# Kernel optimization log

Hardware: AMD Instinct MI355X
Metric: run time of the kernel (lower is better)

## Reference

```python
import jax, jax.numpy as jnp
import numpy as np

B, S, HID, USZ, PSZ, OUT = 128, 512, 768, 200, 200, 200
N_SENT = 16  # 16 sentences of 32 tokens; offsets row = [0,32,...,480,-1]


def setup_inputs() -> dict:
    key = jax.random.key(0)
    ks = jax.random.split(key, 8)
    H = jax.random.normal(ks[0], (B, S, HID), jnp.float32)
    u = jax.random.normal(ks[1], (B, USZ), jnp.float32)
    p = jax.random.normal(ks[2], (B, PSZ), jnp.float32)
    Wh = jax.random.normal(ks[3], (HID, OUT), jnp.float32) * 0.05
    Wu = jax.random.normal(ks[4], (USZ, OUT), jnp.float32) * 0.05
    Wp = jax.random.normal(ks[5], (PSZ, OUT), jnp.float32) * 0.05
    v = jax.random.normal(ks[6], (OUT,), jnp.float32) * 0.05
    b = jnp.zeros((OUT,), jnp.float32)  # torch buffer self.b = zeros
    # offsets: N_SENT sentence starts + trailing -1 sentinel -> [B, N_SENT+1]
    row = jnp.concatenate([jnp.arange(N_SENT, dtype=jnp.int32) * (S // N_SENT),
                           jnp.array([-1], jnp.int32)])
    sentence_offsets = jnp.tile(row[None, :], (B, 1))
    return {"H": H, "u": u, "p": p, "Wh": Wh, "Wu": Wu, "Wp": Wp,
            "v": v, "b": b, "sentence_offsets": sentence_offsets}


def reference(H, u, p, Wh, Wu, Wp, v, b, sentence_offsets):
    # Additive attention scores for every token: v . tanh(Wh H + Wu u + Wp p + b)
    Ht = jnp.einsum('bsh,ho->bso', H, Wh)                      # [B,S,OUT]
    ut = (u @ Wu)[:, None, :]                                  # [B,1,OUT]
    pt = (p @ Wp)[:, None, :]                                  # [B,1,OUT]
    scores = jnp.tanh(Ht + ut + pt + b) @ v                    # [B,S]

    Bsz, Sl, _ = H.shape
    beg = sentence_offsets[:, :-1]                             # [B,M]
    nxt = sentence_offsets[:, 1:]                              # [B,M]
    valid = beg != -1
    # faithful to torch: end = 512 if next==-1 else next-1 (off-by-one kept)
    end = jnp.where(nxt == -1, Sl, nxt - 1)
    t = jnp.arange(Sl)
    mask = valid[:, :, None] & (t[None, None, :] >= beg[:, :, None]) \
           & (t[None, None, :] < end[:, :, None])              # [B,M,S]

    neg_inf = jnp.float32(-jnp.inf)
    em = jnp.where(mask, scores[:, None, :], neg_inf)
    m = jnp.max(em, axis=-1, keepdims=True)
    w = jnp.exp(em - jnp.where(jnp.isfinite(m), m, 0.0)) * mask
    denom = jnp.sum(w, axis=-1, keepdims=True)
    alphas = w / jnp.where(denom > 0, denom, 1.0)              # ragged softmax
    # per-sentence weighted sum of H -> [B, M, HID] (invalid sentences = 0)
    return jnp.einsum('bms,bsh->bmh', alphas, H)
```

## Files before the change

kernel.cpp:

```cpp
#include <hip/hip_runtime.h>
#include <math.h>

#define Bn   128
#define Sn   512
#define HIDn 768
#define OUTn 200
#define MSEG 16
#define NPAD 224
#define NT   14
#define NTW  7
#define KIT  24
#define ROWS 32
#define PH   3
#define KPP  8

typedef __attribute__((ext_vector_type(8))) short short8;
typedef __attribute__((ext_vector_type(4))) float f32x4;

#define GL2LDS(gp, lp) __builtin_amdgcn_global_load_lds(                  \
    (const __attribute__((address_space(1))) void*)(gp),                  \
    (__attribute__((address_space(3))) void*)(lp), 16, 0, 0)

static __device__ inline unsigned short f2bf(float f) {
  union { float f; unsigned u; } v; v.f = f;
  unsigned r = v.u + 0x7FFFu + ((v.u >> 16) & 1u);
  return (unsigned short)(r >> 16);
}

static __device__ inline float fast_tanh(float x) {
  float t = fabsf(x);
  float e = __expf(-2.f * t);
  float r = (1.f - e) * __builtin_amdgcn_rcpf(1.f + e);
  return copysignf(r, x);
}

__global__ __launch_bounds__(256) void setup_kernel(
    const float* __restrict__ Wh, const float* __restrict__ v,
    unsigned short* __restrict__ WhF, float* __restrict__ vP) {
  int idx = blockIdx.x * 256 + threadIdx.x;
  if (blockIdx.x == 0 && threadIdx.x < NPAD)
    vP[threadIdx.x] = (threadIdx.x < OUTn) ? v[threadIdx.x] : 0.f;
  if (idx < NPAD * HIDn) {
    int n = idx / HIDn;
    int k = idx - n * HIDn;
    float val = (n < OUTn) ? Wh[(size_t)k * OUTn + n] : 0.f;
    size_t d = ((size_t)(k >> 5) * NT + (n >> 4)) * 512
             + ((k >> 3) & 3) * 128 + (n & 15) * 8 + (k & 7);
    WhF[d] = f2bf(val);
  }
}

__global__ __launch_bounds__(256) void bias_kernel(
    const float* __restrict__ u, const float* __restrict__ p,
    const float* __restrict__ Wu, const float* __restrict__ Wp,
    const float* __restrict__ bvec, float* __restrict__ biasP) {
  int b = blockIdx.x;
  __shared__ float ul[OUTn], pl[OUTn];
  int tid = threadIdx.x;
  if (tid < OUTn) { ul[tid] = u[b * OUTn + tid]; pl[tid] = p[b * OUTn + tid]; }
  __syncthreads();
  if (tid < NPAD) {
    float s0 = 0.f, s1 = 0.f;
    if (tid < OUTn) {
      s0 = bvec[tid];
      for (int k = 0; k < OUTn; k += 2) {
        s0 += ul[k] * Wu[k * OUTn + tid] + pl[k] * Wp[k * OUTn + tid];
        s1 += ul[k + 1] * Wu[(k + 1) * OUTn + tid] + pl[k + 1] * Wp[(k + 1) * OUTn + tid];
      }
    }
    biasP[(size_t)b * NPAD + tid] = s0 + s1;
  }
}

__global__ __launch_bounds__(256) void fused_kernel(
    const float* __restrict__ H, const unsigned short* __restrict__ WhF,
    const float* __restrict__ biasP, const float* __restrict__ vP,
    const int* __restrict__ offs, float* __restrict__ out) {
  __shared__ float As[2][KPP * 1024];
  __shared__ float scp[2][ROWS];
  __shared__ float o_l[4][HIDn];

  int tid = threadIdx.x, wave = tid >> 6, lane = tid & 63;
  int quad = lane >> 4, l16 = lane & 15;
  int mh = wave >> 1, nh = wave & 1;
  int bid = blockIdx.x;
  int b = bid >> 4;
  int seg = bid & 15;
  int s0 = seg << 5;

  const float* Hblk = H + (size_t)(b * Sn + s0) * HIDn;

  int rloc = lane >> 3;
  int csrc = (lane & 7) ^ (rloc & 7);
  const float* Hst = Hblk + (size_t)rloc * HIDn + csrc * 4;

#define STAGE(ph, bf)                                                        \
  {                                                                          \
    _Pragma("unroll")                                                        \
    for (int t = 0; t < 8; ++t) {                                            \
      int i_ = wave * 8 + t;                                                 \
      int ks_ = i_ >> 2, qt_ = i_ & 3;                                       \
      GL2LDS(Hst + (size_t)(qt_ * 8) * HIDn + ((ph) * KPP + ks_) * 32,       \
             &As[bf][ks_ * 1024 + qt_ * 256]);                               \
    }                                                                        \
  }

  f32x4 acc[NTW];
#pragma unroll
  for (int j = 0; j < NTW; ++j) acc[j] = (f32x4){0.f, 0.f, 0.f, 0.f};

  const short8* Bw = (const short8*)WhF + lane;
  int row = mh * 16 + l16;
  int slot0 = (2 * quad) ^ (l16 & 7);

  STAGE(0, 0);
  __syncthreads();

#pragma unroll
  for (int ph = 0; ph < PH; ++ph) {
    int bf = ph & 1;
#pragma unroll
    for (int ks = 0; ks < KPP; ++ks) {
      int kk = ph * KPP + ks;
      short8 bfr[NTW];
#pragma unroll
      for (int j = 0; j < NTW; ++j)
        bfr[j] = Bw[(kk * NT + nh * NTW + j) * 64];
      if (ks == 2 && ph + 1 < PH) STAGE(ph + 1, bf ^ 1);
      const float* Ab = &As[bf][ks * 1024 + row * 32];
      float4 h0 = *(const float4*)(Ab + slot0 * 4);
      float4 h1 = *(const float4*)(Ab + (slot0 ^ 1) * 4);
      short8 a;
      a[0] = f2bf(h0.x); a[1] = f2bf(h0.y); a[2] = f2bf(h0.z); a[3] = f2bf(h0.w);
      a[4] = f2bf(h1.x); a[5] = f2bf(h1.y); a[6] = f2bf(h1.z); a[7] = f2bf(h1.w);
#pragma unroll
      for (int j = 0; j < NTW; ++j)
        acc[j] = __builtin_amdgcn_mfma_f32_16x16x32_bf16(a, bfr[j], acc[j], 0, 0, 0);
    }
    __syncthreads();
  }

  {
    const float* bp = biasP + (size_t)b * NPAD + nh * (NTW * 16) + l16;
    const float* vp = vP + nh * (NTW * 16) + l16;
    float bv[NTW], vv[NTW];
#pragma unroll
    for (int j = 0; j < NTW; ++j) { bv[j] = bp[j * 16]; vv[j] = vp[j * 16]; }
#pragma unroll
    for (int r = 0; r < 4; ++r) {
      float s = 0.f;
#pragma unroll
      for (int j = 0; j < NTW; ++j)
        s += fast_tanh(acc[j][r] + bv[j]) * vv[j];
      s += __shfl_xor(s, 1); s += __shfl_xor(s, 2);
      s += __shfl_xor(s, 4); s += __shfl_xor(s, 8);
      if (l16 == 0) scp[nh][mh * 16 + quad * 4 + r] = s;
    }
  }
  __syncthreads();

  int beg = offs[b * (MSEG + 1) + seg];
  int nxt = offs[b * (MSEG + 1) + seg + 1];
  bool valid = (beg != -1);
  int end = (nxt == -1) ? Sn : nxt - 1;

  float x = -INFINITY;
  if (lane < 32) {
    int rw = s0 + lane;
    if (valid && rw >= beg && rw < end)
      x = scp[0][lane] + scp[1][lane];
  }
  float mx = x;
  mx = fmaxf(mx, __shfl_xor(mx, 1));  mx = fmaxf(mx, __shfl_xor(mx, 2));
  mx = fmaxf(mx, __shfl_xor(mx, 4));  mx = fmaxf(mx, __shfl_xor(mx, 8));
  mx = fmaxf(mx, __shfl_xor(mx, 16)); mx = fmaxf(mx, __shfl_xor(mx, 32));
  float mm = (mx > -1e30f) ? mx : 0.f;
  float e = __expf(x - mm);
  float ls = e;
  ls += __shfl_xor(ls, 1);  ls += __shfl_xor(ls, 2);
  ls += __shfl_xor(ls, 4);  ls += __shfl_xor(ls, 8);
  ls += __shfl_xor(ls, 16); ls += __shfl_xor(ls, 32);
  float inv = (ls > 0.f) ? 1.f / ls : 0.f;
  float av = e * inv;

  float af[8];
#pragma unroll
  for (int i = 0; i < 8; ++i) af[i] = __shfl(av, wave * 8 + i);

  const float4* Hrow = (const float4*)(H + (size_t)(b * Sn + s0 + wave * 8) * HIDn);
  float4 o0 = {0,0,0,0}, o1 = {0,0,0,0}, o2 = {0,0,0,0};
#pragma unroll
  for (int i = 0; i < 8; ++i) {
    const float4* hp = Hrow + (size_t)i * (HIDn / 4);
    float4 h0 = hp[lane], h1 = hp[lane + 64], h2 = hp[lane + 128];
    float a = af[i];
    o0.x += a * h0.x; o0.y += a * h0.y; o0.z += a * h0.z; o0.w += a * h0.w;
    o1.x += a * h1.x; o1.y += a * h1.y; o1.z += a * h1.z; o1.w += a * h1.w;
    o2.x += a * h2.x; o2.y += a * h2.y; o2.z += a * h2.z; o2.w += a * h2.w;
  }
  {
    float4* ol = (float4*)o_l[wave];
    ol[lane] = o0; ol[lane + 64] = o1; ol[lane + 128] = o2;
  }
  __syncthreads();

  if (tid < 192) {
    const float4* p0 = (const float4*)o_l[0];
    const float4* p1 = (const float4*)o_l[1];
    const float4* p2 = (const float4*)o_l[2];
    const float4* p3 = (const float4*)o_l[3];
    float4 a0 = p0[tid], a1 = p1[tid], a2 = p2[tid], a3 = p3[tid];
    float4 s;
    s.x = a0.x + a1.x + a2.x + a3.x;
    s.y = a0.y + a1.y + a2.y + a3.y;
    s.z = a0.z + a1.z + a2.z + a3.z;
    s.w = a0.w + a1.w + a2.w + a3.w;
    ((float4*)(out + ((size_t)b * MSEG + seg) * HIDn))[tid] = s;
  }
}

extern "C" void kernel_launch(void* const* d_in, const int* in_sizes, int n_in,
                              void* d_out, int out_size, void* d_ws, size_t ws_size,
                              hipStream_t stream) {
  const float* H    = (const float*)d_in[0];
  const float* u    = (const float*)d_in[1];
  const float* p    = (const float*)d_in[2];
  const float* Wh   = (const float*)d_in[3];
  const float* Wu   = (const float*)d_in[4];
  const float* Wp   = (const float*)d_in[5];
  const float* v    = (const float*)d_in[6];
  const float* bvec = (const float*)d_in[7];
  const int*   offs = (const int*)d_in[8];
  float* out = (float*)d_out;

  float* biasP = (float*)d_ws;
  float* vP    = biasP + (size_t)Bn * NPAD;
  unsigned short* WhF = (unsigned short*)(vP + NPAD);

  setup_kernel<<<(NPAD * HIDn + 255) / 256, 256, 0, stream>>>(Wh, v, WhF, vP);
  bias_kernel<<<Bn, 256, 0, stream>>>(u, p, Wu, Wp, bvec, biasP);
  fused_kernel<<<(Bn * Sn) / ROWS, 256, 0, stream>>>(H, WhF, biasP, vP, offs, out);
}
```

Before: 375.6 us.

## Stage H as bf16 in LDS and halve waves, each covering two M-tiles

```diff
diff --git a/kernel.cpp b/kernel.cpp
--- a/kernel.cpp
+++ b/kernel.cpp
@@ -9,17 +9,10 @@
 #define NPAD 224
 #define NT   14
 #define NTW  7
-#define KIT  24
 #define ROWS 32
-#define PH   3
-#define KPP  8
 
 typedef __attribute__((ext_vector_type(8))) short short8;
 typedef __attribute__((ext_vector_type(4))) float f32x4;
-
-#define GL2LDS(gp, lp) __builtin_amdgcn_global_load_lds(                  \
-    (const __attribute__((address_space(1))) void*)(gp),                  \
-    (__attribute__((address_space(3))) void*)(lp), 16, 0, 0)
 
 static __device__ inline unsigned short f2bf(float f) {
   union { float f; unsigned u; } v; v.f = f;
@@ -72,17 +65,17 @@
   }
 }
 
-__global__ __launch_bounds__(256) void fused_kernel(
+__global__ __launch_bounds__(128) void fused_kernel(
     const float* __restrict__ H, const unsigned short* __restrict__ WhF,
     const float* __restrict__ biasP, const float* __restrict__ vP,
     const int* __restrict__ offs, float* __restrict__ out) {
-  __shared__ float As[2][KPP * 1024];
+  __shared__ unsigned short __attribute__((aligned(16))) Abf[ROWS * 384];
   __shared__ float scp[2][ROWS];
-  __shared__ float o_l[4][HIDn];
+  __shared__ float o_l[2][HIDn];
 
   int tid = threadIdx.x, wave = tid >> 6, lane = tid & 63;
   int quad = lane >> 4, l16 = lane & 15;
-  int mh = wave >> 1, nh = wave & 1;
+  int nh = wave;
   int bid = blockIdx.x;
   int b = bid >> 4;
   int seg = bid & 15;
@@ -90,54 +83,64 @@
 
   const float* Hblk = H + (size_t)(b * Sn + s0) * HIDn;
 
-  int rloc = lane >> 3;
-  int csrc = (lane & 7) ^ (rloc & 7);
-  const float* Hst = Hblk + (size_t)rloc * HIDn + csrc * 4;
-
-#define STAGE(ph, bf)                                                        \
-  {                                                                          \
-    _Pragma("unroll")                                                        \
-    for (int t = 0; t < 8; ++t) {                                            \
-      int i_ = wave * 8 + t;                                                 \
-      int ks_ = i_ >> 2, qt_ = i_ & 3;                                       \
-      GL2LDS(Hst + (size_t)(qt_ * 8) * HIDn + ((ph) * KPP + ks_) * 32,       \
-             &As[bf][ks_ * 1024 + qt_ * 256]);                               \
-    }                                                                        \
-  }
-
-  f32x4 acc[NTW];
-#pragma unroll
-  for (int j = 0; j < NTW; ++j) acc[j] = (f32x4){0.f, 0.f, 0.f, 0.f};
+  f32x4 acc[2][NTW];
+#pragma unroll
+  for (int mt = 0; mt < 2; ++mt)
+#pragma unroll
+    for (int j = 0; j < NTW; ++j) acc[mt][j] = (f32x4){0.f, 0.f, 0.f, 0.f};
 
   const short8* Bw = (const short8*)WhF + lane;
-  int row = mh * 16 + l16;
-  int slot0 = (2 * quad) ^ (l16 & 7);
-
-  STAGE(0, 0);
-  __syncthreads();
-
-#pragma unroll
-  for (int ph = 0; ph < PH; ++ph) {
-    int bf = ph & 1;
-#pragma unroll
-    for (int ks = 0; ks < KPP; ++ks) {
-      int kk = ph * KPP + ks;
+
+#define STG_LOAD(R, J0, h)                                                   \
+  { _Pragma("unroll") for (int q = 0; q < 4; ++q) {                          \
+      int d0 = 2 * (((J0) + q) * 128 + tid);                                 \
+      int rw = d0 / 96, cr = d0 - rw * 96;                                   \
+      const float* gp = Hblk + (size_t)rw * HIDn + (h) * 384 + cr * 4;       \
+      R[q][0] = *(const float4*)gp;                                          \
+      R[q][1] = *(const float4*)(gp + 4);                                    \
+  } }
+#define STG_WRITE(R, J0)                                                     \
+  { _Pragma("unroll") for (int q = 0; q < 4; ++q) {                          \
+      int m = ((J0) + q) * 128 + tid;                                        \
+      int rw = m / 48, crb = m - rw * 48;                                    \
+      short8 t;                                                              \
+      t[0] = f2bf(R[q][0].x); t[1] = f2bf(R[q][0].y);                        \
+      t[2] = f2bf(R[q][0].z); t[3] = f2bf(R[q][0].w);                        \
+      t[4] = f2bf(R[q][1].x); t[5] = f2bf(R[q][1].y);                        \
+      t[6] = f2bf(R[q][1].z); t[7] = f2bf(R[q][1].w);                        \
+      *(short8*)&Abf[rw * 384 + ((crb ^ (rw & 7)) << 3)] = t;                \
+  } }
+
+#pragma unroll
+  for (int h = 0; h < 2; ++h) {
+    {
+      float4 rA[4][2], rB[4][2], rC[4][2];
+      STG_LOAD(rA, 0, h);
+      STG_LOAD(rB, 4, h);
+      STG_WRITE(rA, 0);
+      STG_LOAD(rC, 8, h);
+      STG_WRITE(rB, 4);
+      STG_WRITE(rC, 8);
+    }
+    __syncthreads();
+
+#pragma unroll
+    for (int ks = 0; ks < 12; ++ks) {
+      int kk = h * 12 + ks;
       short8 bfr[NTW];
 #pragma unroll
       for (int j = 0; j < NTW; ++j)
         bfr[j] = Bw[(kk * NT + nh * NTW + j) * 64];
-      if (ks == 2 && ph + 1 < PH) STAGE(ph + 1, bf ^ 1);
-      const float* Ab = &As[bf][ks * 1024 + row * 32];
-      float4 h0 = *(const float4*)(Ab + slot0 * 4);
-      float4 h1 = *(const float4*)(Ab + (slot0 ^ 1) * 4);
-      short8 a;
-      a[0] = f2bf(h0.x); a[1] = f2bf(h0.y); a[2] = f2bf(h0.z); a[3] = f2bf(h0.w);
-      a[4] = f2bf(h1.x); a[5] = f2bf(h1.y); a[6] = f2bf(h1.z); a[7] = f2bf(h1.w);
-#pragma unroll
-      for (int j = 0; j < NTW; ++j)
-        acc[j] = __builtin_amdgcn_mfma_f32_16x16x32_bf16(a, bfr[j], acc[j], 0, 0, 0);
-    }
-    __syncthreads();
+      int ca = (((ks << 2) | quad) ^ (l16 & 7)) << 3;
+      short8 a0 = *(const short8*)&Abf[l16 * 384 + ca];
+      short8 a1 = *(const short8*)&Abf[(l16 + 16) * 384 + ca];
+#pragma unroll
+      for (int j = 0; j < NTW; ++j) {
+        acc[0][j] = __builtin_amdgcn_mfma_f32_16x16x32_bf16(a0, bfr[j], acc[0][j], 0, 0, 0);
+        acc[1][j] = __builtin_amdgcn_mfma_f32_16x16x32_bf16(a1, bfr[j], acc[1][j], 0, 0, 0);
+      }
+    }
+    if (h == 0) __syncthreads();
   }
 
   {
@@ -147,15 +150,17 @@
 #pragma unroll
     for (int j = 0; j < NTW; ++j) { bv[j] = bp[j * 16]; vv[j] = vp[j * 16]; }
 #pragma unroll
-    for (int r = 0; r < 4; ++r) {
-      float s = 0.f;
-#pragma unroll
-      for (int j = 0; j < NTW; ++j)
-        s += fast_tanh(acc[j][r] + bv[j]) * vv[j];
-      s += __shfl_xor(s, 1); s += __shfl_xor(s, 2);
-      s += __shfl_xor(s, 4); s += __shfl_xor(s, 8);
-      if (l16 == 0) scp[nh][mh * 16 + quad * 4 + r] = s;
-    }
+    for (int mt = 0; mt < 2; ++mt)
+#pragma unroll
+      for (int r = 0; r < 4; ++r) {
+        float s = 0.f;
+#pragma unroll
+        for (int j = 0; j < NTW; ++j)
+          s += fast_tanh(acc[mt][j][r] + bv[j]) * vv[j];
+        s += __shfl_xor(s, 1); s += __shfl_xor(s, 2);
+        s += __shfl_xor(s, 4); s += __shfl_xor(s, 8);
+        if (l16 == 0) scp[nh][mt * 16 + quad * 4 + r] = s;
+      }
   }
   __syncthreads();
 
@@ -183,14 +188,14 @@
   float inv = (ls > 0.f) ? 1.f / ls : 0.f;
   float av = e * inv;
 
-  float af[8];
-#pragma unroll
-  for (int i = 0; i < 8; ++i) af[i] = __shfl(av, wave * 8 + i);
-
-  const float4* Hrow = (const float4*)(H + (size_t)(b * Sn + s0 + wave * 8) * HIDn);
+  float af[16];
+#pragma unroll
+  for (int i = 0; i < 16; ++i) af[i] = __shfl(av, wave * 16 + i);
+
+  const float4* Hrow = (const float4*)(H + (size_t)(b * Sn + s0 + wave * 16) * HIDn);
   float4 o0 = {0,0,0,0}, o1 = {0,0,0,0}, o2 = {0,0,0,0};
-#pragma unroll
-  for (int i = 0; i < 8; ++i) {
+#pragma unroll 4
+  for (int i = 0; i < 16; ++i) {
     const float4* hp = Hrow + (size_t)i * (HIDn / 4);
     float4 h0 = hp[lane], h1 = hp[lane + 64], h2 = hp[lane + 128];
     float a = af[i];
@@ -204,18 +209,21 @@
   }
   __syncthreads();
 
-  if (tid < 192) {
+  {
     const float4* p0 = (const float4*)o_l[0];
     const float4* p1 = (const float4*)o_l[1];
-    const float4* p2 = (const float4*)o_l[2];
-    const float4* p3 = (const float4*)o_l[3];
-    float4 a0 = p0[tid], a1 = p1[tid], a2 = p2[tid], a3 = p3[tid];
-    float4 s;
-    s.x = a0.x + a1.x + a2.x + a3.x;
-    s.y = a0.y + a1.y + a2.y + a3.y;
-    s.z = a0.z + a1.z + a2.z + a3.z;
-    s.w = a0.w + a1.w + a2.w + a3.w;
-    ((float4*)(out + ((size_t)b * MSEG + seg) * HIDn))[tid] = s;
+    float4* op = (float4*)(out + ((size_t)b * MSEG + seg) * HIDn);
+#pragma unroll
+    for (int base = 0; base < 192; base += 128) {
+      int idx = base + tid;
+      if (idx < 192) {
+        float4 a0 = p0[idx], a1 = p1[idx];
+        float4 s;
+        s.x = a0.x + a1.x; s.y = a0.y + a1.y;
+        s.z = a0.z + a1.z; s.w = a0.w + a1.w;
+        op[idx] = s;
+      }
+    }
   }
 }
 
@@ -239,5 +247,5 @@
 
   setup_kernel<<<(NPAD * HIDn + 255) / 256, 256, 0, stream>>>(Wh, v, WhF, vP);
   bias_kernel<<<Bn, 256, 0, stream>>>(u, p, Wu, Wp, bvec, biasP);
-  fused_kernel<<<(Bn * Sn) / ROWS, 256, 0, stream>>>(H, WhF, biasP, vP, offs, out);
-}
+  fused_kernel<<<(Bn * Sn) / ROWS, 128, 0, stream>>>(H, WhF, biasP, vP, offs, out);
+}
```

Result: slower. 391.7 us (+4.3%).

## Stage H as bf16 in LDS via registers, split N across waves, replicate weights

Applied to the files above, without the earlier changes.

```diff
diff --git a/kernel.cpp b/kernel.cpp
--- a/kernel.cpp
+++ b/kernel.cpp
@@ -6,20 +6,16 @@
 #define HIDn 768
 #define OUTn 200
 #define MSEG 16
-#define NPAD 224
-#define NT   14
-#define NTW  7
-#define KIT  24
+#define NPAD 256
+#define NT   16
+#define NTW  4
+#define NQ   4
+#define KQ   6
 #define ROWS 32
-#define PH   3
-#define KPP  8
+#define NREP 8
 
 typedef __attribute__((ext_vector_type(8))) short short8;
 typedef __attribute__((ext_vector_type(4))) float f32x4;
-
-#define GL2LDS(gp, lp) __builtin_amdgcn_global_load_lds(                  \
-    (const __attribute__((address_space(1))) void*)(gp),                  \
-    (__attribute__((address_space(3))) void*)(lp), 16, 0, 0)
 
 static __device__ inline unsigned short f2bf(float f) {
   union { float f; unsigned u; } v; v.f = f;
@@ -36,7 +32,7 @@
 
 __global__ __launch_bounds__(256) void setup_kernel(
     const float* __restrict__ Wh, const float* __restrict__ v,
-    unsigned short* __restrict__ WhF, float* __restrict__ vP) {
+    unsigned short* __restrict__ WhF, float* __restrict__ vP, int nrep) {
   int idx = blockIdx.x * 256 + threadIdx.x;
   if (blockIdx.x == 0 && threadIdx.x < NPAD)
     vP[threadIdx.x] = (threadIdx.x < OUTn) ? v[threadIdx.x] : 0.f;
@@ -46,7 +42,9 @@
     float val = (n < OUTn) ? Wh[(size_t)k * OUTn + n] : 0.f;
     size_t d = ((size_t)(k >> 5) * NT + (n >> 4)) * 512
              + ((k >> 3) & 3) * 128 + (n & 15) * 8 + (k & 7);
-    WhF[d] = f2bf(val);
+    unsigned short bv = f2bf(val);
+    for (int r = 0; r < nrep; ++r)
+      WhF[(size_t)r * ((size_t)NPAD * HIDn) + d] = bv;
   }
 }
 
@@ -59,30 +57,28 @@
   int tid = threadIdx.x;
   if (tid < OUTn) { ul[tid] = u[b * OUTn + tid]; pl[tid] = p[b * OUTn + tid]; }
   __syncthreads();
-  if (tid < NPAD) {
-    float s0 = 0.f, s1 = 0.f;
-    if (tid < OUTn) {
-      s0 = bvec[tid];
-      for (int k = 0; k < OUTn; k += 2) {
-        s0 += ul[k] * Wu[k * OUTn + tid] + pl[k] * Wp[k * OUTn + tid];
-        s1 += ul[k + 1] * Wu[(k + 1) * OUTn + tid] + pl[k + 1] * Wp[(k + 1) * OUTn + tid];
-      }
-    }
-    biasP[(size_t)b * NPAD + tid] = s0 + s1;
-  }
+  float s0 = 0.f, s1 = 0.f;
+  if (tid < OUTn) {
+    s0 = bvec[tid];
+    for (int k = 0; k < OUTn; k += 2) {
+      s0 += ul[k] * Wu[k * OUTn + tid] + pl[k] * Wp[k * OUTn + tid];
+      s1 += ul[k + 1] * Wu[(k + 1) * OUTn + tid] + pl[k + 1] * Wp[(k + 1) * OUTn + tid];
+    }
+  }
+  biasP[(size_t)b * NPAD + tid] = s0 + s1;
 }
 
 __global__ __launch_bounds__(256) void fused_kernel(
     const float* __restrict__ H, const unsigned short* __restrict__ WhF,
     const float* __restrict__ biasP, const float* __restrict__ vP,
-    const int* __restrict__ offs, float* __restrict__ out) {
-  __shared__ float As[2][KPP * 1024];
-  __shared__ float scp[2][ROWS];
-  __shared__ float o_l[4][HIDn];
+    const int* __restrict__ offs, float* __restrict__ out, int repmask) {
+  __shared__ unsigned char __attribute__((aligned(16))) smraw[ROWS * 192 * 2];
+  __shared__ float scp[4][ROWS];
+  unsigned short* sma = (unsigned short*)smraw;
+  float (*smo)[HIDn] = (float (*)[HIDn])smraw;
 
   int tid = threadIdx.x, wave = tid >> 6, lane = tid & 63;
   int quad = lane >> 4, l16 = lane & 15;
-  int mh = wave >> 1, nh = wave & 1;
   int bid = blockIdx.x;
   int b = bid >> 4;
   int seg = bid & 15;
@@ -90,72 +86,87 @@
 
   const float* Hblk = H + (size_t)(b * Sn + s0) * HIDn;
 
-  int rloc = lane >> 3;
-  int csrc = (lane & 7) ^ (rloc & 7);
-  const float* Hst = Hblk + (size_t)rloc * HIDn + csrc * 4;
-
-#define STAGE(ph, bf)                                                        \
-  {                                                                          \
-    _Pragma("unroll")                                                        \
-    for (int t = 0; t < 8; ++t) {                                            \
-      int i_ = wave * 8 + t;                                                 \
-      int ks_ = i_ >> 2, qt_ = i_ & 3;                                       \
-      GL2LDS(Hst + (size_t)(qt_ * 8) * HIDn + ((ph) * KPP + ks_) * 32,       \
-             &As[bf][ks_ * 1024 + qt_ * 256]);                               \
-    }                                                                        \
-  }
-
-  f32x4 acc[NTW];
-#pragma unroll
-  for (int j = 0; j < NTW; ++j) acc[j] = (f32x4){0.f, 0.f, 0.f, 0.f};
-
-  const short8* Bw = (const short8*)WhF + lane;
-  int row = mh * 16 + l16;
-  int slot0 = (2 * quad) ^ (l16 & 7);
-
-  STAGE(0, 0);
-  __syncthreads();
-
-#pragma unroll
-  for (int ph = 0; ph < PH; ++ph) {
-    int bf = ph & 1;
-#pragma unroll
-    for (int ks = 0; ks < KPP; ++ks) {
-      int kk = ph * KPP + ks;
+  const float* gp_[3]; int ldst_[3];
+#pragma unroll
+  for (int w = 0; w < 3; ++w) {
+    int m = w * 256 + tid;
+    int r = m / 24, c = m - r * 24;
+    gp_[w] = Hblk + (size_t)r * HIDn + c * 8;
+    ldst_[w] = r * 192 + ((c ^ (r & 7)) << 3);
+  }
+
+  f32x4 acc[2][NTW];
+#pragma unroll
+  for (int mt = 0; mt < 2; ++mt)
+#pragma unroll
+    for (int j = 0; j < NTW; ++j) acc[mt][j] = (f32x4){0.f, 0.f, 0.f, 0.f};
+
+  const short8* Bw = (const short8*)(WhF +
+      (size_t)(bid & repmask) * ((size_t)NPAD * HIDn)) + lane;
+
+  float4 R[3][2];
+#pragma unroll
+  for (int w = 0; w < 3; ++w) {
+    R[w][0] = *(const float4*)gp_[w];
+    R[w][1] = *(const float4*)(gp_[w] + 4);
+  }
+
+#pragma unroll
+  for (int p = 0; p < NQ; ++p) {
+#pragma unroll
+    for (int w = 0; w < 3; ++w) {
+      short8 t;
+      t[0] = f2bf(R[w][0].x); t[1] = f2bf(R[w][0].y);
+      t[2] = f2bf(R[w][0].z); t[3] = f2bf(R[w][0].w);
+      t[4] = f2bf(R[w][1].x); t[5] = f2bf(R[w][1].y);
+      t[6] = f2bf(R[w][1].z); t[7] = f2bf(R[w][1].w);
+      *(short8*)&sma[ldst_[w]] = t;
+    }
+    __syncthreads();
+    if (p + 1 < NQ) {
+#pragma unroll
+      for (int w = 0; w < 3; ++w) {
+        R[w][0] = *(const float4*)(gp_[w] + (p + 1) * 192);
+        R[w][1] = *(const float4*)(gp_[w] + (p + 1) * 192 + 4);
+      }
+    }
+#pragma unroll
+    for (int ks = 0; ks < KQ; ++ks) {
+      int kk = p * KQ + ks;
       short8 bfr[NTW];
 #pragma unroll
       for (int j = 0; j < NTW; ++j)
-        bfr[j] = Bw[(kk * NT + nh * NTW + j) * 64];
-      if (ks == 2 && ph + 1 < PH) STAGE(ph + 1, bf ^ 1);
-      const float* Ab = &As[bf][ks * 1024 + row * 32];
-      float4 h0 = *(const float4*)(Ab + slot0 * 4);
-      float4 h1 = *(const float4*)(Ab + (slot0 ^ 1) * 4);
-      short8 a;
-      a[0] = f2bf(h0.x); a[1] = f2bf(h0.y); a[2] = f2bf(h0.z); a[3] = f2bf(h0.w);
-      a[4] = f2bf(h1.x); a[5] = f2bf(h1.y); a[6] = f2bf(h1.z); a[7] = f2bf(h1.w);
-#pragma unroll
-      for (int j = 0; j < NTW; ++j)
-        acc[j] = __builtin_amdgcn_mfma_f32_16x16x32_bf16(a, bfr[j], acc[j], 0, 0, 0);
+        bfr[j] = Bw[(kk * NT + wave * NTW + j) * 64];
+      int cs = (((ks << 2) | quad) ^ (l16 & 7)) << 3;
+      short8 a0 = *(const short8*)&sma[l16 * 192 + cs];
+      short8 a1 = *(const short8*)&sma[(l16 + 16) * 192 + cs];
+#pragma unroll
+      for (int j = 0; j < NTW; ++j) {
+        acc[0][j] = __builtin_amdgcn_mfma_f32_16x16x32_bf16(a0, bfr[j], acc[0][j], 0, 0, 0);
+        acc[1][j] = __builtin_amdgcn_mfma_f32_16x16x32_bf16(a1, bfr[j], acc[1][j], 0, 0, 0);
+      }
     }
     __syncthreads();
   }
 
   {
-    const float* bp = biasP + (size_t)b * NPAD + nh * (NTW * 16) + l16;
-    const float* vp = vP + nh * (NTW * 16) + l16;
+    const float* bp = biasP + (size_t)b * NPAD + wave * 64 + l16;
+    const float* vp = vP + wave * 64 + l16;
     float bv[NTW], vv[NTW];
 #pragma unroll
     for (int j = 0; j < NTW; ++j) { bv[j] = bp[j * 16]; vv[j] = vp[j * 16]; }
 #pragma unroll
-    for (int r = 0; r < 4; ++r) {
-      float s = 0.f;
-#pragma unroll
-      for (int j = 0; j < NTW; ++j)
-        s += fast_tanh(acc[j][r] + bv[j]) * vv[j];
-      s += __shfl_xor(s, 1); s += __shfl_xor(s, 2);
-      s += __shfl_xor(s, 4); s += __shfl_xor(s, 8);
-      if (l16 == 0) scp[nh][mh * 16 + quad * 4 + r] = s;
-    }
+    for (int mt = 0; mt < 2; ++mt)
+#pragma unroll
+      for (int r = 0; r < 4; ++r) {
+        float s = 0.f;
+#pragma unroll
+        for (int j = 0; j < NTW; ++j)
+          s += fast_tanh(acc[mt][j][r] + bv[j]) * vv[j];
+        s += __shfl_xor(s, 1); s += __shfl_xor(s, 2);
+        s += __shfl_xor(s, 4); s += __shfl_xor(s, 8);
+        if (l16 == 0) scp[wave][mt * 16 + quad * 4 + r] = s;
+      }
   }
   __syncthreads();
 
@@ -168,7 +179,7 @@
   if (lane < 32) {
     int rw = s0 + lane;
     if (valid && rw >= beg && rw < end)
-      x = scp[0][lane] + scp[1][lane];
+      x = scp[0][lane] + scp[1][lane] + scp[2][lane] + scp[3][lane];
   }
   float mx = x;
   mx = fmaxf(mx, __shfl_xor(mx, 1));  mx = fmaxf(mx, __shfl_xor(mx, 2));
@@ -199,16 +210,16 @@
     o2.x += a * h2.x; o2.y += a * h2.y; o2.z += a * h2.z; o2.w += a * h2.w;
   }
   {
-    float4* ol = (float4*)o_l[wave];
+    float4* ol = (float4*)smo[wave];
     ol[lane] = o0; ol[lane + 64] = o1; ol[lane + 128] = o2;
   }
   __syncthreads();
 
   if (tid < 192) {
-    const float4* p0 = (const float4*)o_l[0];
-    const float4* p1 = (const float4*)o_l[1];
-    const float4* p2 = (const float4*)o_l[2];
-    const float4* p3 = (const float4*)o_l[3];
+    const float4* p0 = (const float4*)smo[0];
+    const float4* p1 = (const float4*)smo[1];
+    const float4* p2 = (const float4*)smo[2];
+    const float4* p3 = (const float4*)smo[3];
     float4 a0 = p0[tid], a1 = p1[tid], a2 = p2[tid], a3 = p3[tid];
     float4 s;
     s.x = a0.x + a1.x + a2.x + a3.x;
@@ -236,8 +247,12 @@
   float* biasP = (float*)d_ws;
   float* vP    = biasP + (size_t)Bn * NPAD;
   unsigned short* WhF = (unsigned short*)(vP + NPAD);
-
-  setup_kernel<<<(NPAD * HIDn + 255) / 256, 256, 0, stream>>>(Wh, v, WhF, vP);
+  size_t fixed = (size_t)Bn * NPAD * 4 + (size_t)NPAD * 4;
+  size_t whfB  = (size_t)NPAD * HIDn * 2;
+  int nrep = (ws_size >= fixed + (size_t)NREP * whfB) ? NREP : 1;
+  int repmask = nrep - 1;
+
+  setup_kernel<<<(NPAD * HIDn + 255) / 256, 256, 0, stream>>>(Wh, v, WhF, vP, nrep);
   bias_kernel<<<Bn, 256, 0, stream>>>(u, p, Wu, Wp, bvec, biasP);
-  fused_kernel<<<(Bn * Sn) / ROWS, 256, 0, stream>>>(H, WhF, biasP, vP, offs, out);
-}
+  fused_kernel<<<(Bn * Sn) / ROWS, 256, 0, stream>>>(H, WhF, biasP, vP, offs, out, repmask);
+}
```

Measured after the change: 347.4 us. 7.5% less time.
